# Kernel optimization log

Hardware: AMD Instinct MI355X
Metric: run time of the kernel (lower is better)

## Reference

```python
import jax, jax.numpy as jnp
import numpy as np

NUM_HEADS = 12
DIM_HEAD = 32
EMBED_DIM = NUM_HEADS * DIM_HEAD  # 384
EPS = 1e-5


def _channel_layernorm(x, w, b):
    # LayerNorm over channel axis (axis=1) of [B, D, S, L], per spatial position
    mu = jnp.mean(x, axis=1, keepdims=True)
    var = jnp.mean(jnp.square(x - mu), axis=1, keepdims=True)
    xn = (x - mu) / jnp.sqrt(var + EPS)
    return xn * w[None, :, None, None] + b[None, :, None, None]


def _qkv(x, w, b):
    # 1x1 conv == per-position matmul: [3D, D] x [B, D, S, L] -> [B, 3D, S, L]
    B, D, S, L = x.shape
    y = jnp.einsum('od,bdsl->bosl', w, x) + b[None, :, None, None]
    q, k, v = jnp.split(y, 3, axis=1)
    shp = (B, NUM_HEADS, DIM_HEAD, S, L)
    return q.reshape(shp), k.reshape(shp), v.reshape(shp)


def setup_inputs() -> dict:
    key = jax.random.key(0)
    ks = jax.random.split(key, 5)
    B, D, S, L = 1, EMBED_DIM, 128, 256
    x = jax.random.normal(ks[0], (B, D, S, L), dtype=jnp.float32)
    row_w = jax.random.normal(ks[1], (3 * D, D), dtype=jnp.float32) * (D ** -0.5)
    row_b = jax.random.normal(ks[2], (3 * D,), dtype=jnp.float32) * 0.02
    col_w = jax.random.normal(ks[3], (3 * D, D), dtype=jnp.float32) * (D ** -0.5)
    col_b = jax.random.normal(ks[4], (3 * D,), dtype=jnp.float32) * 0.02
    return {
        'x': x,
        'row_w': row_w, 'row_b': row_b,
        'col_w': col_w, 'col_b': col_b,
        'ln1_w': jnp.ones((D,), jnp.float32), 'ln1_b': jnp.zeros((D,), jnp.float32),
        'ln2_w': jnp.ones((D,), jnp.float32), 'ln2_b': jnp.zeros((D,), jnp.float32),
    }


def reference(x, row_w, row_b, col_w, col_b, ln1_w, ln1_b, ln2_w, ln2_b):
    B, D, S, L = x.shape
    # --- row attention (attend across L within each row s) ---
    q, k, v = _qkv(x, row_w, row_b)  # [B,H,C,S,L]
    row_attn = jnp.einsum('bhcsi,bhcsj->bhsij', q, k)  # note: no 1/sqrt(d) scaling (faithful)
    row_attn = jax.nn.softmax(row_attn, axis=-1)
    row_out = jnp.einsum('bhsij,bhdsj->bhdsi', row_attn, v).reshape(B, D, S, L)
    out = _channel_layernorm(x + row_out, ln1_w, ln1_b)
    # --- column attention (attend across S within each column l) ---
    q, k, v = _qkv(out, col_w, col_b)
    col_attn = jnp.einsum('bhcil,bhcjl->bhijl', q, k)
    col_attn = jax.nn.softmax(col_attn, axis=-2)
    col_out = jnp.einsum('bhijl,bhdjl->bhdil', col_attn, v).reshape(B, D, S, L)
    out = _channel_layernorm(out + col_out, ln2_w, ln2_b)
    return out
```

## Files before the change

### kernel.cpp

```cpp
#include <hip/hip_runtime.h>
#include <math.h>

#define DCH 384
#define NH 12
#define CH 32
#define SS 128
#define LL 256
#define NPOS 32768
#define THREE_D 1152

typedef _Float16 f16_t;
typedef _Float16 f16x4 __attribute__((ext_vector_type(4)));
typedef _Float16 f16x8 __attribute__((ext_vector_type(8)));
typedef float f32x4 __attribute__((ext_vector_type(4)));

#define GLD16(gptr, lptr) __builtin_amdgcn_global_load_lds( \
    (const __attribute__((address_space(1))) unsigned int*)(gptr), \
    (__attribute__((address_space(3))) unsigned int*)(lptr), 16, 0, 0)

#define WAVE_LDS_FENCE() __asm__ volatile("s_waitcnt lgkmcnt(0)" ::: "memory")

__global__ __launch_bounds__(256) void conv_w(const float* __restrict__ in,
                                              f16_t* __restrict__ out, int n4) {
    int i = blockIdx.x * 256 + threadIdx.x;
    if (i < n4) {
        float4 v = ((const float4*)in)[i];
        unsigned short u0 = __builtin_bit_cast(unsigned short, (f16_t)v.x);
        unsigned short u1 = __builtin_bit_cast(unsigned short, (f16_t)v.y);
        unsigned short u2 = __builtin_bit_cast(unsigned short, (f16_t)v.z);
        unsigned short u3 = __builtin_bit_cast(unsigned short, (f16_t)v.w);
        uint2 r;
        r.x = (unsigned)u0 | ((unsigned)u1 << 16);
        r.y = (unsigned)u2 | ((unsigned)u3 << 16);
        ((uint2*)out)[i] = r;
    }
}

__global__ __launch_bounds__(256) void conv_xT(const float* __restrict__ in,
                                               f16_t* __restrict__ outp) {
    __shared__ float tile[64][65];
    const int p0 = blockIdx.x * 64;
    const int k0 = blockIdx.y * 64;
    const int tx = threadIdx.x & 63, ty = threadIdx.x >> 6;
#pragma unroll
    for (int i = 0; i < 16; ++i)
        tile[ty * 16 + i][tx] = in[(size_t)(k0 + ty * 16 + i) * NPOS + p0 + tx];
    __syncthreads();
    const int pr = threadIdx.x >> 2;
    const int cg = threadIdx.x & 3;
    union { uint4 v[2]; unsigned int u[8]; } res;
#pragma unroll
    for (int j = 0; j < 8; ++j) {
        unsigned short lo = __builtin_bit_cast(unsigned short, (f16_t)tile[cg * 16 + 2 * j][pr]);
        unsigned short hi = __builtin_bit_cast(unsigned short, (f16_t)tile[cg * 16 + 2 * j + 1][pr]);
        res.u[j] = (unsigned)lo | ((unsigned)hi << 16);
    }
    uint4* dst = (uint4*)&outp[(size_t)(p0 + pr) * DCH + k0 + cg * 16];
    dst[0] = res.v[0];
    dst[1] = res.v[1];
}

__global__ __launch_bounds__(256) void qkv_gemm_f16(
        const f16_t* __restrict__ Wh,
        const float* __restrict__ bias,
        const f16_t* __restrict__ Xp,
        f16_t* __restrict__ Yq, f16_t* __restrict__ Yk, f16_t* __restrict__ Yv)
{
    __shared__ f16_t sha[128 * 32];
    __shared__ f16_t shb[128 * 32];
    const int tid  = threadIdx.x;
    const int lane = tid & 63;
    const int wave = tid >> 6;
    const int ot   = blockIdx.x;
    const int o0 = ot * 128;
    const int p0 = blockIdx.y * 128;
    const int wr = wave >> 1, wc = wave & 1;

    f32x4 acc[4][4] = {};

    const int c0 = wave * 128 + lane;
    const int c1 = c0 + 64;
    const f16_t* ga0 = Wh + (size_t)(o0 + (c0 >> 2)) * DCH + (c0 & 3) * 8;
    const f16_t* ga1 = Wh + (size_t)(o0 + (c1 >> 2)) * DCH + (c1 & 3) * 8;
    const f16_t* gb0 = Xp + (size_t)(p0 + (c0 >> 2)) * DCH + (c0 & 3) * 8;
    const f16_t* gb1 = Xp + (size_t)(p0 + (c1 >> 2)) * DCH + (c1 & 3) * 8;
    f16_t* la0 = sha + (wave * 128) * 8;
    f16_t* la1 = sha + (wave * 128 + 64) * 8;
    f16_t* lb0 = shb + (wave * 128) * 8;
    f16_t* lb1 = shb + (wave * 128 + 64) * 8;

    const int mrow = lane & 15;
    const int kg8  = (lane >> 4) * 8;

    for (int kk = 0; kk < DCH; kk += 32) {
        GLD16(ga0 + kk, la0);
        GLD16(ga1 + kk, la1);
        GLD16(gb0 + kk, lb0);
        GLD16(gb1 + kk, lb1);
        __syncthreads();
        f16x8 af[4], bfr[4];
#pragma unroll
        for (int mi = 0; mi < 4; ++mi)
            af[mi] = *(const f16x8*)(sha + (wr * 64 + mi * 16 + mrow) * 32 + kg8);
#pragma unroll
        for (int ni = 0; ni < 4; ++ni)
            bfr[ni] = *(const f16x8*)(shb + (wc * 64 + ni * 16 + mrow) * 32 + kg8);
#pragma unroll
        for (int mi = 0; mi < 4; ++mi)
#pragma unroll
            for (int ni = 0; ni < 4; ++ni)
                acc[mi][ni] = __builtin_amdgcn_mfma_f32_16x16x32_f16(
                    af[mi], bfr[ni], acc[mi][ni], 0, 0, 0);
        __syncthreads();
    }

    const int col = lane & 15;
    const int rq4 = (lane >> 4) * 4;
    const int qkv = ot / 3;
    const int grp = ot % 3;

    if (qkv < 2) {
        f16_t* Yt = (qkv == 0) ? Yq : Yk;
#pragma unroll
        for (int mi = 0; mi < 4; ++mi) {
            const int h  = grp * 4 + wr * 2 + (mi >> 1);
            const int cb = (mi & 1) * 16 + rq4;
            const int ob = o0 + wr * 64 + mi * 16 + rq4;
            const float b0 = bias[ob], b1 = bias[ob + 1];
            const float b2 = bias[ob + 2], b3 = bias[ob + 3];
#pragma unroll
            for (int ni = 0; ni < 4; ++ni) {
                const int p = p0 + wc * 64 + ni * 16 + col;
                union { uint2 u; f16_t h4[4]; } w;
                w.h4[0] = (f16_t)(acc[mi][ni][0] + b0);
                w.h4[1] = (f16_t)(acc[mi][ni][1] + b1);
                w.h4[2] = (f16_t)(acc[mi][ni][2] + b2);
                w.h4[3] = (f16_t)(acc[mi][ni][3] + b3);
                *(uint2*)(Yt + ((size_t)h * NPOS + p) * CH + cb) = w.u;
            }
        }
    } else {
#pragma unroll
        for (int mi = 0; mi < 4; ++mi) {
#pragma unroll
            for (int r = 0; r < 4; ++r) {
                const int cg = grp * 128 + wr * 64 + mi * 16 + rq4 + r;
                const float br = bias[768 + cg];
#pragma unroll
                for (int ni = 0; ni < 4; ++ni) {
                    const int p = p0 + wc * 64 + ni * 16 + col;
                    Yv[(size_t)cg * NPOS + p] = (f16_t)(acc[mi][ni][r] + br);
                }
            }
        }
    }
}

template <int SEQ, bool XT16>
__global__ __launch_bounds__(256) void mfma_attn(
        const f16_t* __restrict__ Yq, const f16_t* __restrict__ Yk,
        const f16_t* __restrict__ Yv, const void* __restrict__ Xv_,
        float* __restrict__ R)
{
    constexpr int JT  = SEQ / 16;
    constexpr int NIT = SEQ / 64;
    constexpr int PST = SEQ + 8;
    constexpr int VST = SEQ + 8;
    __shared__ f16_t Ks[SEQ * CH];
    __shared__ f16_t Vs[CH * VST];
    __shared__ f16_t pb[4][16 * PST];
    const int tid  = threadIdx.x;
    const int lane = tid & 63;
    const int wave = tid >> 6;
    const int col = lane & 15, quad = lane >> 4;
    const int h = blockIdx.x % NH;
    const size_t pbase = (size_t)(blockIdx.x / NH) * SEQ;

    const f16_t* qg = Yq + ((size_t)h * NPOS + pbase) * CH;
    const f16_t* kg = Yk + ((size_t)h * NPOS + pbase) * CH;
    const f16_t* vg = Yv + (size_t)h * CH * NPOS + pbase;
    f16_t* mypb = pb[wave];

#pragma unroll
    for (int i = 0; i < SEQ / 64; ++i) {
        const int off = (wave * (SEQ / 64) + i) * 512;
        GLD16(kg + off + lane * 8, Ks + off);
    }
    {
        constexpr int CPR = SEQ / 8;
        const int vch = tid % CPR;
        const int vr0 = tid / CPR;
#pragma unroll
        for (int r = vr0; r < CH; r += 256 / CPR)
            *(float4*)(Vs + r * VST + vch * 8) =
                *(const float4*)(vg + (size_t)r * NPOS + vch * 8);
    }
    __syncthreads();

    for (int it = 0; it < NIT; ++it) {
        const int i0 = (wave * NIT + it) * 16;
        const f16x8 qf = *(const f16x8*)(qg + (size_t)(i0 + col) * CH + quad * 8);
        f32x4 st[JT];
#pragma unroll
        for (int mt = 0; mt < JT; ++mt) {
            f16x8 kf = *(const f16x8*)(Ks + (mt * 16 + col) * CH + quad * 8);
            st[mt] = __builtin_amdgcn_mfma_f32_16x16x32_f16(kf, qf, (f32x4){0.f, 0.f, 0.f, 0.f}, 0, 0, 0);
        }
        float sum = 0.f;
#pragma unroll
        for (int mt = 0; mt < JT; ++mt)
#pragma unroll
            for (int r = 0; r < 4; ++r) {
                st[mt][r] = __expf(st[mt][r]);
                sum += st[mt][r];
            }
        sum += __shfl_xor(sum, 16, 64);
        sum += __shfl_xor(sum, 32, 64);
        const float inv = 1.f / sum;
#pragma unroll
        for (int mt = 0; mt < JT; ++mt) {
            union { uint2 u; f16_t h4[4]; } w;
            w.h4[0] = (f16_t)(st[mt][0] * inv);
            w.h4[1] = (f16_t)(st[mt][1] * inv);
            w.h4[2] = (f16_t)(st[mt][2] * inv);
            w.h4[3] = (f16_t)(st[mt][3] * inv);
            *(uint2*)(mypb + col * PST + mt * 16 + quad * 4) = w.u;
        }
        WAVE_LDS_FENCE();

        f32x4 o0a = {0.f, 0.f, 0.f, 0.f}, o0b = {0.f, 0.f, 0.f, 0.f};
        f32x4 o1a = {0.f, 0.f, 0.f, 0.f}, o1b = {0.f, 0.f, 0.f, 0.f};
#pragma unroll
        for (int ks = 0; ks < SEQ / 32; ks += 2) {
            f16x8 pf0 = *(const f16x8*)(mypb + col * PST + ks * 32 + quad * 8);
            f16x8 pf1 = *(const f16x8*)(mypb + col * PST + (ks + 1) * 32 + quad * 8);
            f16x8 va0 = *(const f16x8*)(Vs + col * VST + ks * 32 + quad * 8);
            f16x8 va1 = *(const f16x8*)(Vs + col * VST + (ks + 1) * 32 + quad * 8);
            f16x8 vb0 = *(const f16x8*)(Vs + (16 + col) * VST + ks * 32 + quad * 8);
            f16x8 vb1 = *(const f16x8*)(Vs + (16 + col) * VST + (ks + 1) * 32 + quad * 8);
            o0a = __builtin_amdgcn_mfma_f32_16x16x32_f16(va0, pf0, o0a, 0, 0, 0);
            o0b = __builtin_amdgcn_mfma_f32_16x16x32_f16(va1, pf1, o0b, 0, 0, 0);
            o1a = __builtin_amdgcn_mfma_f32_16x16x32_f16(vb0, pf0, o1a, 0, 0, 0);
            o1b = __builtin_amdgcn_mfma_f32_16x16x32_f16(vb1, pf1, o1b, 0, 0, 0);
        }
        const f32x4 ot0 = o0a + o0b;
        const f32x4 ot1 = o1a + o1b;

        const size_t pos = pbase + i0 + col;
        if constexpr (XT16) {
            const f16_t* Xh = (const f16_t*)Xv_;
            const f16x4 xa = *(const f16x4*)(Xh + pos * DCH + h * CH + quad * 4);
            const f16x4 xb = *(const f16x4*)(Xh + pos * DCH + h * CH + 16 + quad * 4);
#pragma unroll
            for (int r = 0; r < 4; ++r) {
                R[(size_t)(h * CH + quad * 4 + r) * NPOS + pos]      = (float)xa[r] + ot0[r];
                R[(size_t)(h * CH + 16 + quad * 4 + r) * NPOS + pos] = (float)xb[r] + ot1[r];
            }
        } else {
            const float* Xf = (const float*)Xv_;
#pragma unroll
            for (int r = 0; r < 4; ++r) {
                const size_t c0r = (size_t)(h * CH + quad * 4 + r) * NPOS + pos;
                const size_t c1r = (size_t)(h * CH + 16 + quad * 4 + r) * NPOS + pos;
                R[c0r] = Xf[c0r] + ot0[r];
                R[c1r] = Xf[c1r] + ot1[r];
            }
        }
    }
}

__global__ __launch_bounds__(256) void ln_stats(const float* __restrict__ A,
                                                float* __restrict__ mu,
                                                float* __restrict__ rs) {
    __shared__ float ssum[4][64], ssq[4][64];
    const int i = threadIdx.x & 63;
    const int g = threadIdx.x >> 6;
    const int p = blockIdx.x * 64 + i;
    float sum = 0.f, sq = 0.f;
    const float* ap = A + (size_t)(g * 96) * NPOS + p;
#pragma unroll 4
    for (int d = 0; d < 96; ++d) {
        float v = ap[(size_t)d * NPOS];
        sum += v;
        sq += v * v;
    }
    ssum[g][i] = sum;
    ssq[g][i] = sq;
    __syncthreads();
    if (g == 0) {
        float s = ssum[0][i] + ssum[1][i] + ssum[2][i] + ssum[3][i];
        float q = ssq[0][i] + ssq[1][i] + ssq[2][i] + ssq[3][i];
        float m = s * (1.f / DCH);
        float var = q * (1.f / DCH) - m * m;
        mu[p] = m;
        rs[p] = rsqrtf(var + 1e-5f);
    }
}

__global__ __launch_bounds__(256) void norm_xT(
        const float* __restrict__ A, const float* __restrict__ mu,
        const float* __restrict__ rs, const float* __restrict__ w,
        const float* __restrict__ b, f16_t* __restrict__ Xp) {
    __shared__ float tile[64][65];
    const int l0 = (blockIdx.x & 3) * 64;
    const int s  = (blockIdx.x >> 2) & (SS - 1);
    const int k0 = (blockIdx.x >> 9) * 64;
    const int tx = threadIdx.x & 63, ty = threadIdx.x >> 6;
    const int pos0 = s * LL + l0;
#pragma unroll
    for (int i = 0; i < 16; ++i) {
        const int d = k0 + ty * 16 + i;
        float v = A[(size_t)d * NPOS + pos0 + tx];
        tile[ty * 16 + i][tx] = (v - mu[pos0 + tx]) * rs[pos0 + tx] * w[d] + b[d];
    }
    __syncthreads();
    const int pr = threadIdx.x >> 2;
    const int cg = threadIdx.x & 3;
    union { uint4 v[2]; unsigned int u[8]; } res;
#pragma unroll
    for (int j = 0; j < 8; ++j) {
        unsigned short lo = __builtin_bit_cast(unsigned short, (f16_t)tile[cg * 16 + 2 * j][pr]);
        unsigned short hi = __builtin_bit_cast(unsigned short, (f16_t)tile[cg * 16 + 2 * j + 1][pr]);
        res.u[j] = (unsigned)lo | ((unsigned)hi << 16);
    }
    uint4* dst = (uint4*)&Xp[(size_t)((l0 + pr) * SS + s) * DCH + k0 + cg * 16];
    dst[0] = res.v[0];
    dst[1] = res.v[1];
}

__global__ __launch_bounds__(256) void norm_transpose(
        const float* __restrict__ in, const float* __restrict__ mu,
        const float* __restrict__ rs, const float* __restrict__ w,
        const float* __restrict__ b, float* __restrict__ out, int Rr, int Cc) {
    __shared__ float tile[32][33];
    const int ntc = Cc >> 5, ntr = Rr >> 5;
    int tc = blockIdx.x % ntc;
    int tr = (blockIdx.x / ntc) % ntr;
    int d = blockIdx.x / (ntc * ntr);
    int tx = threadIdx.x & 31, ty = threadIdx.x >> 5;
    const float* ip = in + (size_t)d * Rr * Cc;
    float* op = out + (size_t)d * Rr * Cc;
    const float wd = w[d], bd = b[d];
#pragma unroll
    for (int i = 0; i < 32; i += 8) {
        const int r = tr * 32 + ty + i;
        const int c = tc * 32 + tx;
        const int pos = r * Cc + c;
        float v = ip[(size_t)r * Cc + c];
        tile[ty + i][tx] = (v - mu[pos]) * rs[pos] * wd + bd;
    }
    __syncthreads();
#pragma unroll
    for (int i = 0; i < 32; i += 8)
        op[(size_t)(tc * 32 + ty + i) * Rr + tr * 32 + tx] = tile[tx][ty + i];
}

extern "C" void kernel_launch(void* const* d_in, const int* in_sizes, int n_in,
                              void* d_out, int out_size, void* d_ws, size_t ws_size,
                              hipStream_t stream) {
    const float* x     = (const float*)d_in[0];
    const float* row_w = (const float*)d_in[1];
    const float* row_b = (const float*)d_in[2];
    const float* col_w = (const float*)d_in[3];
    const float* col_b = (const float*)d_in[4];
    const float* ln1_w = (const float*)d_in[5];
    const float* ln1_b = (const float*)d_in[6];
    const float* ln2_w = (const float*)d_in[7];
    const float* ln2_b = (const float*)d_in[8];
    float* out = (float*)d_out;

    char* ws = (char*)d_ws;
    const size_t ysz = (size_t)NH * NPOS * CH * 2;
    const size_t abytes = (size_t)DCH * NPOS * 4;
    f16_t* Yq = (f16_t*)ws;
    f16_t* Yk = (f16_t*)(ws + ysz);
    f16_t* Yv = (f16_t*)(ws + 2 * ysz);
    float* A  = (float*)(ws + 3 * ysz);
    f16_t* Xp = (f16_t*)(ws + 3 * ysz + abytes);
    f16_t* Wh = (f16_t*)(ws + 3 * ysz + abytes + ysz);
    float* MU = (float*)(ws + 3 * ysz + abytes + ysz + (1 << 21));
    float* RS = MU + NPOS;

    dim3 ggrid(THREE_D / 128, NPOS / 128);
    const int wn4 = THREE_D * DCH / 4;
    dim3 cgrid(NPOS / 64, DCH / 64);

    conv_w<<<(wn4 + 255) / 256, 256, 0, stream>>>(row_w, Wh, wn4);
    conv_xT<<<cgrid, 256, 0, stream>>>(x, Xp);
    qkv_gemm_f16<<<ggrid, 256, 0, stream>>>(Wh, row_b, Xp, Yq, Yk, Yv);
    mfma_attn<LL, false><<<NH * SS, 256, 0, stream>>>(Yq, Yk, Yv, x, A);
    ln_stats<<<NPOS / 64, 256, 0, stream>>>(A, MU, RS);
    norm_xT<<<(DCH / 64) * SS * (LL / 64), 256, 0, stream>>>(A, MU, RS, ln1_w, ln1_b, Xp);

    conv_w<<<(wn4 + 255) / 256, 256, 0, stream>>>(col_w, Wh, wn4);
    qkv_gemm_f16<<<ggrid, 256, 0, stream>>>(Wh, col_b, Xp, Yq, Yk, Yv);
    mfma_attn<SS, true><<<NH * LL, 256, 0, stream>>>(Yq, Yk, Yv, Xp, A);
    ln_stats<<<NPOS / 64, 256, 0, stream>>>(A, MU, RS);
    norm_transpose<<<DCH * (LL / 32) * (SS / 32), 256, 0, stream>>>(
        A, MU, RS, ln2_w, ln2_b, out, LL, SS);
}
```

Baseline: 366.8 us.

## Double-buffer QKV GEMM LDS tiles and remap blocks across XCDs

The QKV GEMM now keeps two LDS buffers, so the next K-slice's global-to-LDS loads are issued before the MFMA work on the current slice. The aim is to hide global load latency behind compute. It also remaps the block index so consecutive output tiles of one position tile land on the same XCD, which should improve L2 reuse of the activation tile. LDS use doubles, which may lower occupancy, and the one-barrier-per-iteration pattern must still order the buffer reuse correctly.

Result: faster. 351.3 us (-4.2%).

```diff
diff --git a/kernel.cpp b/kernel.cpp
--- a/kernel.cpp
+++ b/kernel.cpp
@@ -66,14 +66,18 @@
         const f16_t* __restrict__ Xp,
         f16_t* __restrict__ Yq, f16_t* __restrict__ Yk, f16_t* __restrict__ Yv)
 {
-    __shared__ f16_t sha[128 * 32];
-    __shared__ f16_t shb[128 * 32];
+    __shared__ f16_t sha[2][128 * 32];
+    __shared__ f16_t shb[2][128 * 32];
     const int tid  = threadIdx.x;
     const int lane = tid & 63;
     const int wave = tid >> 6;
-    const int ot   = blockIdx.x;
+
+    const int hwid = blockIdx.y * 9 + blockIdx.x;
+    const int nid  = (hwid & 7) * 288 + (hwid >> 3);
+    const int ot   = nid % 9;
+    const int pt   = nid / 9;
     const int o0 = ot * 128;
-    const int p0 = blockIdx.y * 128;
+    const int p0 = pt * 128;
     const int wr = wave >> 1, wc = wave & 1;
 
     f32x4 acc[4][4] = {};
@@ -84,27 +88,37 @@
     const f16_t* ga1 = Wh + (size_t)(o0 + (c1 >> 2)) * DCH + (c1 & 3) * 8;
     const f16_t* gb0 = Xp + (size_t)(p0 + (c0 >> 2)) * DCH + (c0 & 3) * 8;
     const f16_t* gb1 = Xp + (size_t)(p0 + (c1 >> 2)) * DCH + (c1 & 3) * 8;
-    f16_t* la0 = sha + (wave * 128) * 8;
-    f16_t* la1 = sha + (wave * 128 + 64) * 8;
-    f16_t* lb0 = shb + (wave * 128) * 8;
-    f16_t* lb1 = shb + (wave * 128 + 64) * 8;
+    const int lofA0 = (wave * 128) * 8;
+    const int lofA1 = (wave * 128 + 64) * 8;
 
     const int mrow = lane & 15;
     const int kg8  = (lane >> 4) * 8;
 
-    for (int kk = 0; kk < DCH; kk += 32) {
-        GLD16(ga0 + kk, la0);
-        GLD16(ga1 + kk, la1);
-        GLD16(gb0 + kk, lb0);
-        GLD16(gb1 + kk, lb1);
-        __syncthreads();
+    GLD16(ga0, &sha[0][lofA0]);
+    GLD16(ga1, &sha[0][lofA1]);
+    GLD16(gb0, &shb[0][lofA0]);
+    GLD16(gb1, &shb[0][lofA1]);
+    __syncthreads();
+
+    constexpr int NK = DCH / 32;
+#pragma unroll
+    for (int t = 0; t < NK; ++t) {
+        const int cur = t & 1;
+        const int nxt = cur ^ 1;
+        if (t < NK - 1) {
+            const int kk = (t + 1) * 32;
+            GLD16(ga0 + kk, &sha[nxt][lofA0]);
+            GLD16(ga1 + kk, &sha[nxt][lofA1]);
+            GLD16(gb0 + kk, &shb[nxt][lofA0]);
+            GLD16(gb1 + kk, &shb[nxt][lofA1]);
+        }
         f16x8 af[4], bfr[4];
 #pragma unroll
         for (int mi = 0; mi < 4; ++mi)
-            af[mi] = *(const f16x8*)(sha + (wr * 64 + mi * 16 + mrow) * 32 + kg8);
+            af[mi] = *(const f16x8*)(&sha[cur][(wr * 64 + mi * 16 + mrow) * 32 + kg8]);
 #pragma unroll
         for (int ni = 0; ni < 4; ++ni)
-            bfr[ni] = *(const f16x8*)(shb + (wc * 64 + ni * 16 + mrow) * 32 + kg8);
+            bfr[ni] = *(const f16x8*)(&shb[cur][(wc * 64 + ni * 16 + mrow) * 32 + kg8]);
 #pragma unroll
         for (int mi = 0; mi < 4; ++mi)
 #pragma unroll
```
